# Performance work log

Hardware: AMD Instinct MI355X
Metric: run time of the kernel (lower is better)

## Reference

```python
import jax, jax.numpy as jnp
import numpy as np

# NF4 codebook (from bitsandbytes/torchao)
NF4 = jnp.array([
    -1.0, -0.6961928009986877, -0.5250730514526367, -0.39491748809814453,
    -0.28444138169288635, -0.18477343022823334, -0.09105003625154495, 0.0,
    0.07958029955625534, 0.16093020141124725, 0.24611230194568634,
    0.33791524171829224, 0.44070982933044434, 0.5626170039176941,
    0.7229568362236023, 1.0], dtype=jnp.float32)

IN_DIM, OUT_DIM = 4096, 4096
RANK, ALPHA = 16, 32.0
BLOCK = 64            # nf4 quantization block size
SCALER_BLOCK = 256    # double-quantization block size for scalers


def setup_inputs() -> dict:
    key = jax.random.key(0)
    kx, kw, ka, kb = jax.random.split(key, 4)
    x = jax.random.normal(kx, (4, 2048, IN_DIM), jnp.float32)
    # float base weight, then quantize to NF4 with double-quantized scalers
    w = jax.random.normal(kw, (OUT_DIM, IN_DIM), jnp.float32) * 0.02
    blocks = w.reshape(-1, BLOCK)                          # [n_blocks, 64]
    scalers = jnp.max(jnp.abs(blocks), axis=1)             # per-block absmax
    scaler_mean = jnp.mean(scalers, keepdims=True)         # [1]
    sc = (scalers - scaler_mean).reshape(-1, SCALER_BLOCK) # [n_sblocks, 256]
    q_factor = 127.0 / jnp.max(jnp.abs(sc), axis=1)        # [n_sblocks]
    q_scalers = jnp.clip(jnp.round(sc * q_factor[:, None]), -127, 127)
    q_scalers = q_scalers.astype(jnp.int32).reshape(-1)    # [n_blocks]
    # map normalized values to nearest NF4 code via bucket midpoints
    norm = blocks / scalers[:, None]
    mid = (NF4[:-1] + NF4[1:]) * 0.5
    nf4_idx = jnp.searchsorted(mid, norm).astype(jnp.int32)  # [n_blocks, 64]
    # LoRA weights (kaiming-uniform-like)
    lora_a_w = jax.random.uniform(ka, (RANK, IN_DIM), jnp.float32, -1.0, 1.0) / jnp.sqrt(IN_DIM)
    lora_b_w = jax.random.uniform(kb, (OUT_DIM, RANK), jnp.float32, -1.0, 1.0) / jnp.sqrt(RANK)
    return dict(x=x, nf4_idx=nf4_idx, q_scalers=q_scalers, q_factor=q_factor,
                scaler_mean=scaler_mean, lora_a_w=lora_a_w, lora_b_w=lora_b_w)


def _dequant_nf4(nf4_idx, q_scalers, q_factor, scaler_mean):
    # dequantize double-quantized scalers, then blocks
    scalers = q_scalers.astype(jnp.float32) / jnp.repeat(q_factor, SCALER_BLOCK) + scaler_mean[0]
    w = NF4[nf4_idx] * scalers[:, None]                    # [n_blocks, 64]
    return w.reshape(OUT_DIM, IN_DIM)


def reference(x, nf4_idx, q_scalers, q_factor, scaler_mean, lora_a_w, lora_b_w):
    w = _dequant_nf4(nf4_idx, q_scalers, q_factor, scaler_mean)  # [out, in]
    base = jnp.einsum('bsd,od->bso', x, w)
    # dropout p=0.0 -> identity
    lora = jnp.einsum('bsr,or->bso', jnp.einsum('bsd,rd->bsr', x, lora_a_w), lora_b_w)
    return base + (ALPHA / RANK) * lora
```

## Files before the change

kernel.cpp:

```cpp
#include <hip/hip_runtime.h>
#include <hip/hip_bf16.h>

typedef unsigned short u16;
typedef u16 u16x4 __attribute__((ext_vector_type(4)));
typedef __bf16 bf16x8 __attribute__((ext_vector_type(8)));
typedef float f32x4 __attribute__((ext_vector_type(4)));

#define IN_DIM 4096
#define OUT_DIM 4096
#define M_TOT 8192

__device__ __constant__ float NF4_LUT[16] = {
    -1.0f, -0.6961928009986877f, -0.5250730514526367f, -0.39491748809814453f,
    -0.28444138169288635f, -0.18477343022823334f, -0.09105003625154495f, 0.0f,
    0.07958029955625534f, 0.16093020141124725f, 0.24611230194568634f,
    0.33791524171829224f, 0.44070982933044434f, 0.5626170039176941f,
    0.7229568362236023f, 1.0f};

__device__ __forceinline__ u16 f2bf(float f) {
  unsigned i = __float_as_uint(f);
  i += 0x7fffu + ((i >> 16) & 1u);
  return (u16)(i >> 16);
}

__global__ __launch_bounds__(256) void convert_x(
    const float4* __restrict__ xin, u16x4* __restrict__ xout, int n4)
{
  int i = blockIdx.x * 256 + threadIdx.x;
  const int stride = gridDim.x * 256;
  for (; i < n4; i += stride) {
    const float4 v = xin[i];
    u16x4 o;
    o.x = f2bf(v.x); o.y = f2bf(v.y); o.z = f2bf(v.z); o.w = f2bf(v.w);
    xout[i] = o;
  }
}

__global__ __launch_bounds__(256) void dequant_fold(
    const int* __restrict__ nf4_idx, const int* __restrict__ q_scalers,
    const float* __restrict__ q_factor, const float* __restrict__ scaler_mean,
    const float* __restrict__ lora_a, const float* __restrict__ lora_b,
    u16* __restrict__ w_eff)
{
  __shared__ float s_lut[16];
  __shared__ float s_b[16];
  __shared__ float s_scl[64];
  const int t = threadIdx.x;
  const int o = blockIdx.x;
  if (t < 16) {
    s_lut[t] = NF4_LUT[t];
    s_b[t] = 2.0f * lora_b[o * 16 + t];
  }
  if (t < 64) {
    const int b = o * 64 + t;
    s_scl[t] = (float)q_scalers[b] / q_factor[b >> 8] + scaler_mean[0];
  }
  __syncthreads();

  float Bf[16];
#pragma unroll
  for (int r = 0; r < 16; ++r) Bf[r] = s_b[r];

#pragma unroll
  for (int it = 0; it < 4; ++it) {
    const int d0 = it * 1024 + t * 4;
    const int4 iv = *(const int4*)(nf4_idx + (size_t)o * IN_DIM + d0);
    const float sc = s_scl[d0 >> 6];
    float l0 = 0.f, l1 = 0.f, l2 = 0.f, l3 = 0.f;
#pragma unroll
    for (int r = 0; r < 16; ++r) {
      const float4 av = *(const float4*)(lora_a + (size_t)r * IN_DIM + d0);
      const float br = Bf[r];
      l0 += br * av.x;
      l1 += br * av.y;
      l2 += br * av.z;
      l3 += br * av.w;
    }
    u16x4 ov;
    ov.x = f2bf(s_lut[iv.x] * sc + l0);
    ov.y = f2bf(s_lut[iv.y] * sc + l1);
    ov.z = f2bf(s_lut[iv.z] * sc + l2);
    ov.w = f2bf(s_lut[iv.w] * sc + l3);
    *(u16x4*)(w_eff + (size_t)o * IN_DIM + d0) = ov;
  }
}

#define BM 256
#define BN 256
#define BK 64
#define NT (IN_DIM / BK)

__device__ __forceinline__ void async16(const u16* g, const u16* l) {
  __builtin_amdgcn_global_load_lds(
      (const __attribute__((address_space(1))) void*)g,
      (__attribute__((address_space(3))) void*)l,
      16, 0, 0);
}

#define STG(c, kt, j) do {                                                     \
    async16(gA + (size_t)(j) * 64 * IN_DIM + (kt),                             \
            &sA[(c) * BM * BK + ((j) * 512 + wid * 64) * 8]);                  \
    async16(gB + (size_t)(j) * 64 * IN_DIM + (kt),                             \
            &sB[(c) * BN * BK + ((j) * 512 + wid * 64) * 8]);                  \
  } while (0)

#define MFMA_Q(AF, BF, MI0) do {                                               \
    _Pragma("unroll") for (int mi = (MI0); mi < (MI0) + 4; ++mi)               \
    _Pragma("unroll") for (int ni = 0; ni < 4; ++ni)                           \
      acc[mi][ni] = __builtin_amdgcn_mfma_f32_16x16x32_bf16(                   \
          AF[mi], BF[ni], acc[mi][ni], 0, 0, 0);                               \
  } while (0)

#define KTILE(c, ktn, DOSTAGE, ENDVM_STR, DOENDBAR) do {                       \
                        \
  _Pragma("unroll") for (int mi = 0; mi < 8; ++mi)                             \
    a0[mi] = *(const bf16x8*)&sA[(c) * BM * BK + aBase + mi * 1024 + e0];      \
  _Pragma("unroll") for (int ni = 0; ni < 4; ++ni)                             \
    b0[ni] = *(const bf16x8*)&sB[(c) * BN * BK + bBase + ni * 1024 + e0];      \
  __builtin_amdgcn_s_barrier();                                                \
  asm volatile("s_waitcnt lgkmcnt(0)" ::: "memory");                           \
  __builtin_amdgcn_s_setprio(1);                                               \
  MFMA_Q(a0, b0, 0);                                                           \
  __builtin_amdgcn_s_setprio(0);                                               \
  __builtin_amdgcn_s_barrier();                                                \
                        \
  _Pragma("unroll") for (int mi = 0; mi < 8; ++mi)                             \
    a1[mi] = *(const bf16x8*)&sA[(c) * BM * BK + aBase + mi * 1024 + e1];      \
  _Pragma("unroll") for (int ni = 0; ni < 4; ++ni)                             \
    b1[ni] = *(const bf16x8*)&sB[(c) * BN * BK + bBase + ni * 1024 + e1];      \
  __builtin_amdgcn_s_barrier();                                                \
  asm volatile("s_waitcnt lgkmcnt(0)" ::: "memory");                           \
  __builtin_amdgcn_s_setprio(1);                                               \
  MFMA_Q(a0, b0, 4);                                                           \
  __builtin_amdgcn_s_setprio(0);                                               \
  __builtin_amdgcn_s_barrier();                                                \
                   \
  if (DOSTAGE) { STG(c, ktn, 0); STG(c, ktn, 1); }                             \
  __builtin_amdgcn_s_barrier();                                                \
  __builtin_amdgcn_s_setprio(1);                                               \
  MFMA_Q(a1, b1, 0);                                                           \
  __builtin_amdgcn_s_setprio(0);                                               \
  __builtin_amdgcn_s_barrier();                                                \
                \
  if (DOSTAGE) { STG(c, ktn, 2); STG(c, ktn, 3); }                             \
  __builtin_amdgcn_s_barrier();                                                \
  __builtin_amdgcn_s_setprio(1);                                               \
  MFMA_Q(a1, b1, 4);                                                           \
  __builtin_amdgcn_s_setprio(0);                                               \
  asm volatile("s_waitcnt " ENDVM_STR ::: "memory");                           \
  if (DOENDBAR) __builtin_amdgcn_s_barrier();                                  \
} while (0)

__global__ __launch_bounds__(512, 2) void gemm256(
    const u16* __restrict__ X, const u16* __restrict__ W,
    float* __restrict__ Out)
{
  __shared__ __align__(16) u16 sA[2 * BM * BK];
  __shared__ __align__(16) u16 sB[2 * BN * BK];

  const int tid = threadIdx.x;
  const int lane = tid & 63;
  const int wid = tid >> 6;
  const int wm = wid >> 2;
  const int wn = wid & 3;

  const int bid = blockIdx.x;
  const int swzb = (bid & 7) * 64 + (bid >> 3);
  const int tileM = swzb >> 4;
  const int tileN = swzb & 15;
  const int rowBase = tileM * BM;
  const int colBase = tileN * BN;

  const int cr = tid >> 3;
  const int cq = tid & 7;
  const int qsw = cq ^ (cr & 7);
  const u16* gA = X + (size_t)(rowBase + cr) * IN_DIM + qsw * 8;
  const u16* gB = W + (size_t)(colBase + cr) * IN_DIM + qsw * 8;

  const int l15 = lane & 15;
  const int qhi = lane >> 4;
  const int l7 = lane & 7;
  const int e0 = (qhi ^ l7) * 8;
  const int e1 = ((4 + qhi) ^ l7) * 8;
  const int aBase = (wm * 128 + l15) * 64;
  const int bBase = (wn * 64 + l15) * 64;

  f32x4 acc[8][4] = {};
  bf16x8 a0[8], a1[8], b0[4], b1[4];

  STG(0, 0, 0); STG(0, 0, 1); STG(0, 0, 2); STG(0, 0, 3);
  STG(1, BK, 0); STG(1, BK, 1); STG(1, BK, 2); STG(1, BK, 3);
  asm volatile("s_waitcnt vmcnt(8)" ::: "memory");
  __builtin_amdgcn_s_barrier();

  int kt2 = 2 * BK;
  for (int t = 0; t < NT - 2; t += 2) {
    KTILE(0, kt2, true, "vmcnt(8)", true);
    KTILE(1, kt2 + BK, true, "vmcnt(8)", true);
    kt2 += 2 * BK;
  }
  KTILE(0, 0, false, "vmcnt(0)", true);
  KTILE(1, 0, false, "vmcnt(0)", false);

  const int or4 = qhi * 4;
#pragma unroll
  for (int mi = 0; mi < 8; ++mi) {
#pragma unroll
    for (int i = 0; i < 4; ++i) {
      const size_t r = (size_t)(rowBase + wm * 128 + mi * 16 + or4 + i);
      float* po = Out + r * OUT_DIM + colBase + wn * 64 + l15;
#pragma unroll
      for (int ni = 0; ni < 4; ++ni)
        po[ni * 16] = acc[mi][ni][i];
    }
  }
}

extern "C" void kernel_launch(void* const* d_in, const int* in_sizes, int n_in,
                              void* d_out, int out_size, void* d_ws, size_t ws_size,
                              hipStream_t stream) {
  const float* x         = (const float*)d_in[0];
  const int* nf4_idx     = (const int*)d_in[1];
  const int* q_scalers   = (const int*)d_in[2];
  const float* q_factor  = (const float*)d_in[3];
  const float* scaler_mean = (const float*)d_in[4];
  const float* lora_a    = (const float*)d_in[5];
  const float* lora_b    = (const float*)d_in[6];
  float* out = (float*)d_out;

  const size_t xbf_bytes = (size_t)M_TOT * IN_DIM * sizeof(u16);
  const size_t wef_bytes = (size_t)OUT_DIM * IN_DIM * sizeof(u16);
  if (ws_size < xbf_bytes + wef_bytes) return;
  u16* xbf   = (u16*)d_ws;
  u16* w_eff = (u16*)((char*)d_ws + xbf_bytes);

  hipLaunchKernelGGL(convert_x, dim3(8192), dim3(256), 0, stream,
                     (const float4*)x, (u16x4*)xbf, M_TOT * IN_DIM / 4);
  hipLaunchKernelGGL(dequant_fold, dim3(OUT_DIM), dim3(256), 0, stream,
                     nf4_idx, q_scalers, q_factor, scaler_mean, lora_a, lora_b,
                     w_eff);
  hipLaunchKernelGGL(gemm256, dim3((M_TOT / BM) * (OUT_DIM / BN)), dim3(512),
                     0, stream, xbf, w_eff, out);
}
```

Measured before the change: 569.1 us.

## Switch GEMM to 32x32x16 MFMA and batch four rows per dequant block

The main GEMM moves from 16x16x32 to 32x32x16 bf16 MFMA tiles. All LDS fragments for a K-tile are loaded up front, the schedule collapses into two MFMA phases, and all four global-to-LDS stages are issued after the second phase, with a new epilogue matching the 32x32 output layout. Separately, the dequant+LoRA-fold kernel now handles four output rows per block, so each lora_a load is reused across four rows. The aims are fewer LDS fragment reads per MFMA, fewer barriers, and less redundant lora_a traffic, at the cost of more register pressure and less overlap between global staging and compute.

```diff
diff --git a/kernel.cpp b/kernel.cpp
--- a/kernel.cpp
+++ b/kernel.cpp
@@ -5,6 +5,7 @@
 typedef u16 u16x4 __attribute__((ext_vector_type(4)));
 typedef __bf16 bf16x8 __attribute__((ext_vector_type(8)));
 typedef float f32x4 __attribute__((ext_vector_type(4)));
+typedef float f32x16 __attribute__((ext_vector_type(16)));
 
 #define IN_DIM 4096
 #define OUT_DIM 4096
@@ -43,45 +44,54 @@
     u16* __restrict__ w_eff)
 {
   __shared__ float s_lut[16];
-  __shared__ float s_b[16];
-  __shared__ float s_scl[64];
+  __shared__ float s_b[4][16];
+  __shared__ float s_scl[4][64];
   const int t = threadIdx.x;
-  const int o = blockIdx.x;
-  if (t < 16) {
-    s_lut[t] = NF4_LUT[t];
-    s_b[t] = 2.0f * lora_b[o * 16 + t];
-  }
+  const int o0 = blockIdx.x * 4;
+  if (t < 16) s_lut[t] = NF4_LUT[t];
   if (t < 64) {
-    const int b = o * 64 + t;
-    s_scl[t] = (float)q_scalers[b] / q_factor[b >> 8] + scaler_mean[0];
+    const int row = t >> 4, r = t & 15;
+    s_b[row][r] = 2.0f * lora_b[(o0 + row) * 16 + r];
+  }
+  {
+    const int row = t >> 6, blk = t & 63;
+    const int b = (o0 + row) * 64 + blk;
+    s_scl[row][blk] = (float)q_scalers[b] / q_factor[b >> 8] + scaler_mean[0];
   }
   __syncthreads();
-
-  float Bf[16];
-#pragma unroll
-  for (int r = 0; r < 16; ++r) Bf[r] = s_b[r];
 
 #pragma unroll
   for (int it = 0; it < 4; ++it) {
     const int d0 = it * 1024 + t * 4;
-    const int4 iv = *(const int4*)(nf4_idx + (size_t)o * IN_DIM + d0);
-    const float sc = s_scl[d0 >> 6];
-    float l0 = 0.f, l1 = 0.f, l2 = 0.f, l3 = 0.f;
+    float4 lacc[4];
+#pragma unroll
+    for (int row = 0; row < 4; ++row) {
+      lacc[row].x = 0.f; lacc[row].y = 0.f; lacc[row].z = 0.f; lacc[row].w = 0.f;
+    }
 #pragma unroll
     for (int r = 0; r < 16; ++r) {
       const float4 av = *(const float4*)(lora_a + (size_t)r * IN_DIM + d0);
-      const float br = Bf[r];
-      l0 += br * av.x;
-      l1 += br * av.y;
-      l2 += br * av.z;
-      l3 += br * av.w;
-    }
-    u16x4 ov;
-    ov.x = f2bf(s_lut[iv.x] * sc + l0);
-    ov.y = f2bf(s_lut[iv.y] * sc + l1);
-    ov.z = f2bf(s_lut[iv.z] * sc + l2);
-    ov.w = f2bf(s_lut[iv.w] * sc + l3);
-    *(u16x4*)(w_eff + (size_t)o * IN_DIM + d0) = ov;
+#pragma unroll
+      for (int row = 0; row < 4; ++row) {
+        const float br = s_b[row][r];
+        lacc[row].x += br * av.x;
+        lacc[row].y += br * av.y;
+        lacc[row].z += br * av.z;
+        lacc[row].w += br * av.w;
+      }
+    }
+#pragma unroll
+    for (int row = 0; row < 4; ++row) {
+      const int o = o0 + row;
+      const int4 iv = *(const int4*)(nf4_idx + (size_t)o * IN_DIM + d0);
+      const float sc = s_scl[row][d0 >> 6];
+      u16x4 ov;
+      ov.x = f2bf(s_lut[iv.x] * sc + lacc[row].x);
+      ov.y = f2bf(s_lut[iv.y] * sc + lacc[row].y);
+      ov.z = f2bf(s_lut[iv.z] * sc + lacc[row].z);
+      ov.w = f2bf(s_lut[iv.w] * sc + lacc[row].w);
+      *(u16x4*)(w_eff + (size_t)o * IN_DIM + d0) = ov;
+    }
   }
 }
 
@@ -104,51 +114,41 @@
             &sB[(c) * BN * BK + ((j) * 512 + wid * 64) * 8]);                  \
   } while (0)
 
-#define MFMA_Q(AF, BF, MI0) do {                                               \
-    _Pragma("unroll") for (int mi = (MI0); mi < (MI0) + 4; ++mi)               \
-    _Pragma("unroll") for (int ni = 0; ni < 4; ++ni)                           \
-      acc[mi][ni] = __builtin_amdgcn_mfma_f32_16x16x32_bf16(                   \
-          AF[mi], BF[ni], acc[mi][ni], 0, 0, 0);                               \
+#define MFMA16x32(AF, BF) do {                                                 \
+    _Pragma("unroll") for (int mt = 0; mt < 4; ++mt)                           \
+    _Pragma("unroll") for (int nt = 0; nt < 2; ++nt)                           \
+    _Pragma("unroll") for (int kk = 0; kk < 2; ++kk)                           \
+      acc[mt][nt] = __builtin_amdgcn_mfma_f32_32x32x16_bf16(                   \
+          AF[mt][kk], BF[nt][kk], acc[mt][nt], 0, 0, 0);                       \
   } while (0)
 
-#define KTILE(c, ktn, DOSTAGE, ENDVM_STR, DOENDBAR) do {                       \
+#define KTILE32(c, ktn, DOSTAGE, DOVM, VMSTR) do {                             \
                         \
-  _Pragma("unroll") for (int mi = 0; mi < 8; ++mi)                             \
-    a0[mi] = *(const bf16x8*)&sA[(c) * BM * BK + aBase + mi * 1024 + e0];      \
-  _Pragma("unroll") for (int ni = 0; ni < 4; ++ni)                             \
-    b0[ni] = *(const bf16x8*)&sB[(c) * BN * BK + bBase + ni * 1024 + e0];      \
-  __builtin_amdgcn_s_barrier();                                                \
-  asm volatile("s_waitcnt lgkmcnt(0)" ::: "memory");                           \
-  __builtin_amdgcn_s_setprio(1);                                               \
-  MFMA_Q(a0, b0, 0);                                                           \
-  __builtin_amdgcn_s_setprio(0);                                               \
-  __builtin_amdgcn_s_barrier();                                                \
-                        \
-  _Pragma("unroll") for (int mi = 0; mi < 8; ++mi)                             \
-    a1[mi] = *(const bf16x8*)&sA[(c) * BM * BK + aBase + mi * 1024 + e1];      \
-  _Pragma("unroll") for (int ni = 0; ni < 4; ++ni)                             \
-    b1[ni] = *(const bf16x8*)&sB[(c) * BN * BK + bBase + ni * 1024 + e1];      \
-  __builtin_amdgcn_s_barrier();                                                \
-  asm volatile("s_waitcnt lgkmcnt(0)" ::: "memory");                           \
-  __builtin_amdgcn_s_setprio(1);                                               \
-  MFMA_Q(a0, b0, 4);                                                           \
-  __builtin_amdgcn_s_setprio(0);                                               \
-  __builtin_amdgcn_s_barrier();                                                \
-                   \
-  if (DOSTAGE) { STG(c, ktn, 0); STG(c, ktn, 1); }                             \
+  _Pragma("unroll") for (int mt = 0; mt < 4; ++mt)                             \
+  _Pragma("unroll") for (int kk = 0; kk < 2; ++kk)                             \
+    a0[mt][kk] = *(const bf16x8*)&sA[(c) * BM * BK + aBase + mt * 2048 + eK[kk]];\
+  _Pragma("unroll") for (int nt = 0; nt < 2; ++nt)                             \
+  _Pragma("unroll") for (int kk = 0; kk < 2; ++kk)                             \
+    b0[nt][kk] = *(const bf16x8*)&sB[(c) * BN * BK + bBase + nt * 2048 + eK[kk]];\
+  _Pragma("unroll") for (int mt = 0; mt < 4; ++mt)                             \
+  _Pragma("unroll") for (int kk = 0; kk < 2; ++kk)                             \
+    a1[mt][kk] = *(const bf16x8*)&sA[(c) * BM * BK + aBase + mt * 2048 + eK[2 + kk]];\
+  _Pragma("unroll") for (int nt = 0; nt < 2; ++nt)                             \
+  _Pragma("unroll") for (int kk = 0; kk < 2; ++kk)                             \
+    b1[nt][kk] = *(const bf16x8*)&sB[(c) * BN * BK + bBase + nt * 2048 + eK[2 + kk]];\
   __builtin_amdgcn_s_barrier();                                                \
   __builtin_amdgcn_s_setprio(1);                                               \
-  MFMA_Q(a1, b1, 0);                                                           \
+  MFMA16x32(a0, b0);                          \
   __builtin_amdgcn_s_setprio(0);                                               \
-  __builtin_amdgcn_s_barrier();                                                \
-                \
-  if (DOSTAGE) { STG(c, ktn, 2); STG(c, ktn, 3); }                             \
-  __builtin_amdgcn_s_barrier();                                                \
+  asm volatile("s_waitcnt lgkmcnt(0)" ::: "memory");                           \
+  __builtin_amdgcn_s_barrier();              \
+       \
   __builtin_amdgcn_s_setprio(1);                                               \
-  MFMA_Q(a1, b1, 4);                                                           \
+  MFMA16x32(a1, b1);                                                           \
   __builtin_amdgcn_s_setprio(0);                                               \
-  asm volatile("s_waitcnt " ENDVM_STR ::: "memory");                           \
-  if (DOENDBAR) __builtin_amdgcn_s_barrier();                                  \
+  if (DOSTAGE) { STG(c, ktn, 0); STG(c, ktn, 1); STG(c, ktn, 2); STG(c, ktn, 3); }\
+  if (DOVM) { asm volatile("s_waitcnt " VMSTR ::: "memory"); }                 \
+  __builtin_amdgcn_s_barrier();   \
 } while (0)
 
 __global__ __launch_bounds__(512, 2) void gemm256(
@@ -177,16 +177,18 @@
   const u16* gA = X + (size_t)(rowBase + cr) * IN_DIM + qsw * 8;
   const u16* gB = W + (size_t)(colBase + cr) * IN_DIM + qsw * 8;
 
-  const int l15 = lane & 15;
-  const int qhi = lane >> 4;
+  const int l31 = lane & 31;
+  const int khalf = lane >> 5;
   const int l7 = lane & 7;
-  const int e0 = (qhi ^ l7) * 8;
-  const int e1 = ((4 + qhi) ^ l7) * 8;
-  const int aBase = (wm * 128 + l15) * 64;
-  const int bBase = (wn * 64 + l15) * 64;
-
-  f32x4 acc[8][4] = {};
-  bf16x8 a0[8], a1[8], b0[4], b1[4];
+  int eK[4];
+#pragma unroll
+  for (int kk = 0; kk < 4; ++kk)
+    eK[kk] = ((kk * 2 + khalf) ^ l7) * 8;
+  const int aBase = (wm * 128 + l31) * 64;
+  const int bBase = (wn * 64 + l31) * 64;
+
+  f32x16 acc[4][2] = {};
+  bf16x8 a0[4][2], a1[4][2], b0[2][2], b1[2][2];
 
   STG(0, 0, 0); STG(0, 0, 1); STG(0, 0, 2); STG(0, 0, 3);
   STG(1, BK, 0); STG(1, BK, 1); STG(1, BK, 2); STG(1, BK, 3);
@@ -195,23 +197,23 @@
 
   int kt2 = 2 * BK;
   for (int t = 0; t < NT - 2; t += 2) {
-    KTILE(0, kt2, true, "vmcnt(8)", true);
-    KTILE(1, kt2 + BK, true, "vmcnt(8)", true);
+    KTILE32(0, kt2, true, true, "vmcnt(8)");
+    KTILE32(1, kt2 + BK, true, true, "vmcnt(8)");
     kt2 += 2 * BK;
   }
-  KTILE(0, 0, false, "vmcnt(0)", true);
-  KTILE(1, 0, false, "vmcnt(0)", false);
-
-  const int or4 = qhi * 4;
-#pragma unroll
-  for (int mi = 0; mi < 8; ++mi) {
-#pragma unroll
-    for (int i = 0; i < 4; ++i) {
-      const size_t r = (size_t)(rowBase + wm * 128 + mi * 16 + or4 + i);
-      float* po = Out + r * OUT_DIM + colBase + wn * 64 + l15;
-#pragma unroll
-      for (int ni = 0; ni < 4; ++ni)
-        po[ni * 16] = acc[mi][ni][i];
+  KTILE32(0, 0, false, true, "vmcnt(0)");
+  KTILE32(1, 0, false, false, "vmcnt(0)");
+
+#pragma unroll
+  for (int mt = 0; mt < 4; ++mt) {
+#pragma unroll
+    for (int nt = 0; nt < 2; ++nt) {
+#pragma unroll
+      for (int r = 0; r < 16; ++r) {
+        const int rloc = (r & 3) + 8 * (r >> 2) + 4 * khalf;
+        const size_t row = (size_t)(rowBase + wm * 128 + mt * 32 + rloc);
+        Out[row * OUT_DIM + colBase + wn * 64 + nt * 32 + l31] = acc[mt][nt][r];
+      }
     }
   }
 }
@@ -236,7 +238,7 @@
 
   hipLaunchKernelGGL(convert_x, dim3(8192), dim3(256), 0, stream,
                      (const float4*)x, (u16x4*)xbf, M_TOT * IN_DIM / 4);
-  hipLaunchKernelGGL(dequant_fold, dim3(OUT_DIM), dim3(256), 0, stream,
+  hipLaunchKernelGGL(dequant_fold, dim3(OUT_DIM / 4), dim3(256), 0, stream,
                      nf4_idx, q_scalers, q_factor, scaler_mean, lora_a, lora_b,
                      w_eff);
   hipLaunchKernelGGL(gemm256, dim3((M_TOT / BM) * (OUT_DIM / BN)), dim3(512),
```

New measurement: 616.8 us. 8.4% more time.
